# Performance work log

Measured on AMD Instinct MI355X. Metric: run time of the kernel, lower is better.

## Reference

```python
import jax, jax.numpy as jnp
import numpy as np

# Dimensions: B volumes, S=15 slices, C=16 channels, H=W=6 spatial (hardcoded in module)
B, S, C, H, W = 4096, 15, 16, 6, 6
N_LUNG, N_HEART = 28, 27
N_OUT = 2 * N_LUNG + N_HEART  # 83
IN_FEAT = C * H * W           # 576


def setup_inputs() -> dict:
    key = jax.random.key(0)
    k0, k1, k2, k3, k4 = jax.random.split(key, 5)
    x = jax.random.normal(k0, (B, S, C, H, W), dtype=jnp.float32)
    dzfeatweights_heart = jax.random.normal(k1, (1, N_HEART, C, 1, 1), dtype=jnp.float32)
    dzfeatweights_lung = jax.random.normal(k2, (1, N_LUNG, C, 1, 1), dtype=jnp.float32)
    bound = 1.0 / np.sqrt(IN_FEAT)  # kaiming/fan_in style init bound
    fclayers_weights = jax.random.uniform(k3, (N_OUT, IN_FEAT), minval=-bound, maxval=bound, dtype=jnp.float32)
    fclayers_biases = jax.random.uniform(k4, (N_OUT,), minval=-bound, maxval=bound, dtype=jnp.float32)
    return {"x": x,
            "dzfeatweights_heart": dzfeatweights_heart,
            "dzfeatweights_lung": dzfeatweights_lung,
            "fclayers_weights": fclayers_weights,
            "fclayers_biases": fclayers_biases}


def reference(x, dzfeatweights_heart, dzfeatweights_lung, fclayers_weights, fclayers_biases):
    # x: [B, S, C, H, W] post-backbone features (one row per CT volume)
    Bc, Sc, Cc, Hc, Wc = x.shape
    # nonlinearity='softmax' -> Softmax(dim=2), i.e. over the 16 channels
    attn_heart = jax.nn.softmax(dzfeatweights_heart[0, :, :, 0, 0], axis=1)  # [n_heart, C]
    attn_lung = jax.nn.softmax(dzfeatweights_lung[0, :, :, 0, 0], axis=1)    # [n_lung, C]
    # disease order in the original cat: heart, left lung, right lung (lung weights shared)
    attn = jnp.concatenate([attn_heart, attn_lung, attn_lung], axis=0)       # [O, C]
    # Fuse the channel-attention broadcast-mul into the per-disease FC weights:
    # pred[b,s,o] = sum_{c,h,w} x[b,s,c,h,w] * attn[o,c] * Wfc[o,c,h,w] + bias[o]
    Wfc = fclayers_weights.reshape(-1, Cc, Hc, Wc)                           # [O, C, H, W]
    Weff = attn[:, :, None, None] * Wfc                                      # [O, C, H, W]
    slice_preds = jnp.einsum('bschw,ochw->bso', x, Weff) + fclayers_biases   # [B, S, O]
    # AvgPool1d(kernel_size=slices) over the slice axis -> [B, O]
    return jnp.mean(slice_preds, axis=1)
```

## Files before the change

kernel.cpp:

```cpp
#include <hip/hip_runtime.h>

#define NOUT 83
#define NHEART 27
#define NLUNG 28

typedef float v4f __attribute__((ext_vector_type(4)));

#define GLOAD(dst, ptr, offs) \
    asm volatile("global_load_dwordx4 %0, %1, off offset:" offs \
                 : "=v"(dst) : "v"(ptr))

__global__ __launch_bounds__(512) void bodyavg_scan8f(
    const v4f* __restrict__ x4,
    const float* __restrict__ dzh,
    const float* __restrict__ dzl,
    const v4f* __restrict__ fcw4,
    const float* __restrict__ fcb,
    float* __restrict__ out,
    int B)
{
    __shared__ float attn_lds[NOUT * 17];
    __shared__ v4f   xms[8 * 144];

    const int tid = threadIdx.x;
    const int blk = blockIdx.x;
    const int b0  = blk * 8;

    const int w = tid >> 6;
    const int l = tid & 63;
    const int b = b0 + w;

    v4f acc[9];
    #pragma unroll
    for (int j = 0; j < 9; ++j) acc[j] = (v4f){0.f, 0.f, 0.f, 0.f};

    if (b < B) {
        const v4f* src = x4 + (size_t)b * 2160 + l;
        const v4f* p0 = src;
        const v4f* p1 = src + 256;
        const v4f* p2 = src + 512;

        #pragma unroll
        for (int c = 0; c < 3; ++c) {
            v4f t0, t1, t2, t3, t4, t5, t6, t7, t8;
            GLOAD(t0, p0, "0");    GLOAD(t1, p0, "1024");
            GLOAD(t2, p0, "2048"); GLOAD(t3, p0, "3072");
            GLOAD(t4, p1, "0");    GLOAD(t5, p1, "1024");
            GLOAD(t6, p1, "2048"); GLOAD(t7, p1, "3072");
            GLOAD(t8, p2, "0");
            asm volatile("s_waitcnt vmcnt(4)" ::: "memory");
            __builtin_amdgcn_sched_barrier(0);
            acc[0] += t0; acc[1] += t1; acc[2] += t2; acc[3] += t3; acc[4] += t4;
            asm volatile("s_waitcnt vmcnt(0)" ::: "memory");
            __builtin_amdgcn_sched_barrier(0);
            acc[5] += t5; acc[6] += t6; acc[7] += t7; acc[8] += t8;
            p0 += 576; p1 += 576; p2 += 576;
        }
        {
            v4f t0, t1, t2, t3, t4, t5;
            GLOAD(t0, p0, "0");    GLOAD(t1, p0, "1024");
            GLOAD(t2, p0, "2048"); GLOAD(t3, p0, "3072");
            GLOAD(t4, p1, "0");    GLOAD(t5, p1, "1024");
            asm volatile("s_waitcnt vmcnt(0)" ::: "memory");
            __builtin_amdgcn_sched_barrier(0);
            acc[0] += t0; acc[1] += t1; acc[2] += t2;
            acc[3] += t3; acc[4] += t4; acc[5] += t5;
        }
        if (l < 48) acc[6] += src[2112];
    }

    {
        const v4f z = (v4f){0.f, 0.f, 0.f, 0.f};
        xms[w * 144 + l] = z;
        xms[w * 144 + 64 + l] = z;
        if (l < 16) xms[w * 144 + 128 + l] = z;
    }
    #pragma unroll
    for (int j = 0; j < 9; ++j) {
        int p = (64 * j) % 144 + l;
        if (p >= 144) p -= 144;
        xms[w * 144 + p] += acc[j];
    }

    if (tid < NOUT) {
        const int o = tid;
        const float* row = (o < NHEART) ? (dzh + o * 16)
                                        : (dzl + ((o - NHEART) % NLUNG) * 16);
        float vals[16];
        #pragma unroll
        for (int c = 0; c < 16; ++c) vals[c] = row[c];
        float m = vals[0];
        #pragma unroll
        for (int c = 1; c < 16; ++c) m = fmaxf(m, vals[c]);
        float s = 0.f;
        #pragma unroll
        for (int c = 0; c < 16; ++c) { vals[c] = expf(vals[c] - m); s += vals[c]; }
        const float inv = (1.0f / s) * (1.0f / 15.0f);
        #pragma unroll
        for (int c = 0; c < 16; ++c) attn_lds[o * 17 + c] = vals[c] * inv;
    }

    __syncthreads();

    const int grp = tid >> 4;
    const int ll  = tid & 15;

    int oc[3];
    const v4f* wr[3];
    #pragma unroll
    for (int k = 0; k < 3; ++k) {
        const int o = grp + 32 * k;
        oc[k] = (o < NOUT) ? o : 0;
        wr[k] = fcw4 + oc[k] * 144;
    }

    float facc[3][8] = {};

    #pragma unroll 3
    for (int jj = 0; jj < 9; ++jj) {
        const int q  = ll + 16 * jj;
        const int cc = q / 9;

        v4f xv[8];
        #pragma unroll
        for (int v = 0; v < 8; ++v) xv[v] = xms[v * 144 + q];

        #pragma unroll
        for (int k = 0; k < 3; ++k) {
            const v4f  wq = wr[k][q];
            const float a = attn_lds[oc[k] * 17 + cc];
            const float wx = a * wq.x, wy = a * wq.y, wz = a * wq.z, ww = a * wq.w;
            #pragma unroll
            for (int v = 0; v < 8; ++v) {
                facc[k][v] = fmaf(wx, xv[v].x, facc[k][v]);
                facc[k][v] = fmaf(wy, xv[v].y, facc[k][v]);
                facc[k][v] = fmaf(wz, xv[v].z, facc[k][v]);
                facc[k][v] = fmaf(ww, xv[v].w, facc[k][v]);
            }
        }
    }

    #pragma unroll
    for (int k = 0; k < 3; ++k) {
        float r4[4];
        #pragma unroll
        for (int j = 0; j < 4; ++j) {
            const float lo = facc[k][2 * j], hi = facc[k][2 * j + 1];
            const bool  up = (ll & 1);
            const float keep = up ? hi : lo;
            const float send = up ? lo : hi;
            r4[j] = keep + __shfl_xor(send, 1, 16);
        }
        float r2[2];
        #pragma unroll
        for (int j = 0; j < 2; ++j) {
            const float lo = r4[2 * j], hi = r4[2 * j + 1];
            const bool  up = (ll & 2);
            const float keep = up ? hi : lo;
            const float send = up ? lo : hi;
            r2[j] = keep + __shfl_xor(send, 2, 16);
        }
        float r1;
        {
            const float lo = r2[0], hi = r2[1];
            const bool  up = (ll & 4);
            const float keep = up ? hi : lo;
            const float send = up ? lo : hi;
            r1 = keep + __shfl_xor(send, 4, 16);
        }
        r1 += __shfl_xor(r1, 8, 16);

        const int o = grp + 32 * k;
        const int bb = b0 + (ll & 7);
        if (ll < 8 && o < NOUT && bb < B)
            out[(size_t)bb * NOUT + o] = r1 + fcb[o];
    }
}

extern "C" void kernel_launch(void* const* d_in, const int* in_sizes, int n_in,
                              void* d_out, int out_size, void* d_ws, size_t ws_size,
                              hipStream_t stream) {
    const float* x   = (const float*)d_in[0];
    const float* dzh = (const float*)d_in[1];
    const float* dzl = (const float*)d_in[2];
    const float* fcw = (const float*)d_in[3];
    const float* fcb = (const float*)d_in[4];
    float* out = (float*)d_out;

    const int B = in_sizes[0] / (15 * 16 * 6 * 6);
    const int blocks = (B + 7) / 8;

    hipLaunchKernelGGL(bodyavg_scan8f, dim3(blocks), dim3(512), 0, stream,
                       reinterpret_cast<const v4f*>(x), dzh, dzl,
                       reinterpret_cast<const v4f*>(fcw), fcb, out, B);
}
```

Before: 35.69 us.

## Split each volume's slice stream across two waves with rolling LDS accumulation

Doubles the block to 1024 threads so two waves share each volume, each streaming half of the slice data. Each wave keeps a rolling window of eight in-flight loads and accumulates straight into its own LDS region, replacing the batched load-then-add pattern with register accumulators. The two partial sums are added when read in the FC stage, which now has 64 groups covering outputs with two per thread instead of three. The aim is more memory-level parallelism per CU for this bandwidth-bound read. In exchange it adds LDS read-modify-write traffic and larger blocks that may limit how many blocks are resident per CU.

```diff
diff --git a/kernel.cpp b/kernel.cpp
--- a/kernel.cpp
+++ b/kernel.cpp
@@ -10,7 +10,46 @@
     asm volatile("global_load_dwordx4 %0, %1, off offset:" offs \
                  : "=v"(dst) : "v"(ptr))
 
-__global__ __launch_bounds__(512) void bodyavg_scan8f(
+#define WAITV(lit) \
+    asm volatile("s_waitcnt vmcnt(" lit ")" ::: "memory"); \
+    __builtin_amdgcn_sched_barrier(0)
+
+constexpr int kPOS[9] = {0, 64, 128, 48, 112, 32, 96, 16, 80};
+
+#define DRAIN(u, lit) { \
+    int p = kPOS[(u) % 9] + l; if (p >= 144) p -= 144; \
+    v4f cur = region[p]; \
+    asm volatile("s_waitcnt vmcnt(" lit ")" ::: "memory"); \
+    __builtin_amdgcn_sched_barrier(0); \
+    region[p] = cur + t[(u) & 7]; }
+
+template<int NFULL>
+__device__ __forceinline__ void stream_half(const v4f* srcq, v4f* region, int l)
+{
+    v4f t[8];
+    const v4f* pA = srcq;
+    const v4f* pB = srcq + 256;
+    GLOAD(t[0], pA, "0");    GLOAD(t[1], pA, "1024");
+    GLOAD(t[2], pA, "2048"); GLOAD(t[3], pA, "3072");
+    GLOAD(t[4], pB, "0");    GLOAD(t[5], pB, "1024");
+    GLOAD(t[6], pB, "2048"); GLOAD(t[7], pB, "3072");
+    const v4f* P = srcq + 512;
+
+    #pragma unroll
+    for (int u = 0; u <= NFULL - 9; ++u) {
+        int p = kPOS[u % 9] + l; if (p >= 144) p -= 144;
+        v4f cur = region[p];
+        WAITV("7");
+        region[p] = cur + t[u & 7];
+        GLOAD(t[u & 7], P, "0");
+        P += 64;
+    }
+    constexpr int D0 = NFULL - 8;
+    DRAIN(D0 + 0, "7"); DRAIN(D0 + 1, "6"); DRAIN(D0 + 2, "5"); DRAIN(D0 + 3, "4");
+    DRAIN(D0 + 4, "3"); DRAIN(D0 + 5, "2"); DRAIN(D0 + 6, "1"); DRAIN(D0 + 7, "0");
+}
+
+__global__ __launch_bounds__(1024) void bodyavg_hilo(
     const v4f* __restrict__ x4,
     const float* __restrict__ dzh,
     const float* __restrict__ dzl,
@@ -20,7 +59,7 @@
     int B)
 {
     __shared__ float attn_lds[NOUT * 17];
-    __shared__ v4f   xms[8 * 144];
+    __shared__ v4f   xms[16][144];
 
     const int tid = threadIdx.x;
     const int blk = blockIdx.x;
@@ -28,58 +67,28 @@
 
     const int w = tid >> 6;
     const int l = tid & 63;
-    const int b = b0 + w;
-
-    v4f acc[9];
-    #pragma unroll
-    for (int j = 0; j < 9; ++j) acc[j] = (v4f){0.f, 0.f, 0.f, 0.f};
+    const int v = w >> 1;
+    const int h = w & 1;
+    const int b = b0 + v;
+
+    v4f* region = xms[w];
+    {
+        const v4f z = {0.f, 0.f, 0.f, 0.f};
+        region[l] = z; region[64 + l] = z;
+        if (l < 16) region[128 + l] = z;
+    }
 
     if (b < B) {
-        const v4f* src = x4 + (size_t)b * 2160 + l;
-        const v4f* p0 = src;
-        const v4f* p1 = src + 256;
-        const v4f* p2 = src + 512;
-
-        #pragma unroll
-        for (int c = 0; c < 3; ++c) {
-            v4f t0, t1, t2, t3, t4, t5, t6, t7, t8;
-            GLOAD(t0, p0, "0");    GLOAD(t1, p0, "1024");
-            GLOAD(t2, p0, "2048"); GLOAD(t3, p0, "3072");
-            GLOAD(t4, p1, "0");    GLOAD(t5, p1, "1024");
-            GLOAD(t6, p1, "2048"); GLOAD(t7, p1, "3072");
-            GLOAD(t8, p2, "0");
-            asm volatile("s_waitcnt vmcnt(4)" ::: "memory");
-            __builtin_amdgcn_sched_barrier(0);
-            acc[0] += t0; acc[1] += t1; acc[2] += t2; acc[3] += t3; acc[4] += t4;
-            asm volatile("s_waitcnt vmcnt(0)" ::: "memory");
-            __builtin_amdgcn_sched_barrier(0);
-            acc[5] += t5; acc[6] += t6; acc[7] += t7; acc[8] += t8;
-            p0 += 576; p1 += 576; p2 += 576;
-        }
-        {
-            v4f t0, t1, t2, t3, t4, t5;
-            GLOAD(t0, p0, "0");    GLOAD(t1, p0, "1024");
-            GLOAD(t2, p0, "2048"); GLOAD(t3, p0, "3072");
-            GLOAD(t4, p1, "0");    GLOAD(t5, p1, "1024");
-            asm volatile("s_waitcnt vmcnt(0)" ::: "memory");
-            __builtin_amdgcn_sched_barrier(0);
-            acc[0] += t0; acc[1] += t1; acc[2] += t2;
-            acc[3] += t3; acc[4] += t4; acc[5] += t5;
-        }
-        if (l < 48) acc[6] += src[2112];
-    }
-
-    {
-        const v4f z = (v4f){0.f, 0.f, 0.f, 0.f};
-        xms[w * 144 + l] = z;
-        xms[w * 144 + 64 + l] = z;
-        if (l < 16) xms[w * 144 + 128 + l] = z;
-    }
-    #pragma unroll
-    for (int j = 0; j < 9; ++j) {
-        int p = (64 * j) % 144 + l;
-        if (p >= 144) p -= 144;
-        xms[w * 144 + p] += acc[j];
+        const v4f* srcq = x4 + (size_t)b * 2160 + h * 1152 + l;
+        if (h == 0) {
+            stream_half<18>(srcq, region, l);
+        } else {
+            stream_half<15>(srcq, region, l);
+            if (l < 48) {
+                const v4f tt = srcq[960];
+                region[96 + l] += tt;
+            }
+        }
     }
 
     if (tid < NOUT) {
@@ -105,43 +114,45 @@
     const int grp = tid >> 4;
     const int ll  = tid & 15;
 
-    int oc[3];
-    const v4f* wr[3];
+    int oc[2];
+    const v4f* wr[2];
     #pragma unroll
-    for (int k = 0; k < 3; ++k) {
-        const int o = grp + 32 * k;
+    for (int k = 0; k < 2; ++k) {
+        const int o = grp + 64 * k;
         oc[k] = (o < NOUT) ? o : 0;
         wr[k] = fcw4 + oc[k] * 144;
     }
 
-    float facc[3][8] = {};
+    float facc[2][8] = {};
 
     #pragma unroll 3
     for (int jj = 0; jj < 9; ++jj) {
         const int q  = ll + 16 * jj;
         const int cc = q / 9;
 
-        v4f xv[8];
-        #pragma unroll
-        for (int v = 0; v < 8; ++v) xv[v] = xms[v * 144 + q];
-
-        #pragma unroll
-        for (int k = 0; k < 3; ++k) {
-            const v4f  wq = wr[k][q];
-            const float a = attn_lds[oc[k] * 17 + cc];
-            const float wx = a * wq.x, wy = a * wq.y, wz = a * wq.z, ww = a * wq.w;
-            #pragma unroll
-            for (int v = 0; v < 8; ++v) {
-                facc[k][v] = fmaf(wx, xv[v].x, facc[k][v]);
-                facc[k][v] = fmaf(wy, xv[v].y, facc[k][v]);
-                facc[k][v] = fmaf(wz, xv[v].z, facc[k][v]);
-                facc[k][v] = fmaf(ww, xv[v].w, facc[k][v]);
-            }
+        const v4f  wq0 = wr[0][q];
+        const v4f  wq1 = wr[1][q];
+        const float a0 = attn_lds[oc[0] * 17 + cc];
+        const float a1 = attn_lds[oc[1] * 17 + cc];
+        const float s0x = a0 * wq0.x, s0y = a0 * wq0.y, s0z = a0 * wq0.z, s0w = a0 * wq0.w;
+        const float s1x = a1 * wq1.x, s1y = a1 * wq1.y, s1z = a1 * wq1.z, s1w = a1 * wq1.w;
+
+        #pragma unroll
+        for (int vv = 0; vv < 8; ++vv) {
+            const v4f xv = xms[2 * vv][q] + xms[2 * vv + 1][q];
+            facc[0][vv] = fmaf(s0x, xv.x, facc[0][vv]);
+            facc[0][vv] = fmaf(s0y, xv.y, facc[0][vv]);
+            facc[0][vv] = fmaf(s0z, xv.z, facc[0][vv]);
+            facc[0][vv] = fmaf(s0w, xv.w, facc[0][vv]);
+            facc[1][vv] = fmaf(s1x, xv.x, facc[1][vv]);
+            facc[1][vv] = fmaf(s1y, xv.y, facc[1][vv]);
+            facc[1][vv] = fmaf(s1z, xv.z, facc[1][vv]);
+            facc[1][vv] = fmaf(s1w, xv.w, facc[1][vv]);
         }
     }
 
     #pragma unroll
-    for (int k = 0; k < 3; ++k) {
+    for (int k = 0; k < 2; ++k) {
         float r4[4];
         #pragma unroll
         for (int j = 0; j < 4; ++j) {
@@ -170,7 +181,7 @@
         }
         r1 += __shfl_xor(r1, 8, 16);
 
-        const int o = grp + 32 * k;
+        const int o  = grp + 64 * k;
         const int bb = b0 + (ll & 7);
         if (ll < 8 && o < NOUT && bb < B)
             out[(size_t)bb * NOUT + o] = r1 + fcb[o];
@@ -190,7 +201,7 @@
     const int B = in_sizes[0] / (15 * 16 * 6 * 6);
     const int blocks = (B + 7) / 8;
 
-    hipLaunchKernelGGL(bodyavg_scan8f, dim3(blocks), dim3(512), 0, stream,
+    hipLaunchKernelGGL(bodyavg_hilo, dim3(blocks), dim3(1024), 0, stream,
                        reinterpret_cast<const v4f*>(x), dzh, dzl,
                        reinterpret_cast<const v4f*>(fcw), fcb, out, B);
 }
```

New measurement: 38.14 us. +6.9%, slower.
